# Kernel tuning notes

Measured on AMD Instinct MI355X. Metric: run time of the kernel, lower is better.

Reference implementation:

```python
import jax, jax.numpy as jnp
import numpy as np

WS = 8      # window size
S = 2       # num_heads
GRID = jnp.linspace(-2.0, 2.0, 8)  # RBF grid, num_grids=8
DENOM = 4.0 / 7.0                  # (grid_max-grid_min)/(num_grids-1)


def _layernorm(x, g, b, eps=1e-5):
    mu = x.mean(-1, keepdims=True)
    var = ((x - mu) ** 2).mean(-1, keepdims=True)
    return (x - mu) * jax.lax.rsqrt(var + eps) * g + b


def _fastkan(x, ln_g, ln_b, ws, wb, bb):
    # x: (..., in_dim). RBF basis: (..., in_dim, 8) -> flatten -> spline GEMM; plus SiLU base path.
    ln = _layernorm(x, ln_g, ln_b)
    basis = jnp.exp(-(((ln[..., None] - GRID) / DENOM) ** 2))
    flat = basis.reshape(*basis.shape[:-2], -1)
    return flat @ ws.T + jax.nn.silu(x) @ wb.T + bb


def setup_inputs() -> dict:
    key = jax.random.key(0)
    ks = jax.random.split(key, 16)
    d = {
        'x': jax.random.normal(ks[0], (4, 32, 256, 256), dtype=jnp.float32),
        'pn_g': jnp.ones((32,), jnp.float32), 'pn_b': jnp.zeros((32,), jnp.float32),
        'k1_ln_g': jnp.ones((16,), jnp.float32), 'k1_ln_b': jnp.zeros((16,), jnp.float32),
        'k1_ws': jax.random.normal(ks[1], (16, 128), jnp.float32) * 0.1,
        'k1_wb': jax.random.normal(ks[2], (16, 16), jnp.float32) * 0.1,
        'k1_bb': jnp.zeros((16,), jnp.float32),
        'k2_ln_g': jnp.ones((16,), jnp.float32), 'k2_ln_b': jnp.zeros((16,), jnp.float32),
        'k2_ws': jax.random.normal(ks[3], (16, 128), jnp.float32) * 0.1,
        'k2_wb': jax.random.normal(ks[4], (16, 16), jnp.float32) * 0.1,
        'k2_bb': jnp.zeros((16,), jnp.float32),
        'k3_ln_g': jnp.ones((32,), jnp.float32), 'k3_ln_b': jnp.zeros((32,), jnp.float32),
        'k3_ws': jax.random.normal(ks[5], (32, 256), jnp.float32) * 0.1,
        'k3_wb': jax.random.normal(ks[6], (32, 32), jnp.float32) * 0.1,
        'k3_bb': jnp.zeros((32,), jnp.float32),
        'k4_ln_g': jnp.ones((32,), jnp.float32), 'k4_ln_b': jnp.zeros((32,), jnp.float32),
        'k4_ws': jax.random.normal(ks[7], (32, 256), jnp.float32) * 0.1,
        'k4_wb': jax.random.normal(ks[8], (32, 32), jnp.float32) * 0.1,
        'k4_bb': jnp.zeros((32,), jnp.float32),
    }
    return d


def reference(x, pn_g, pn_b,
              k1_ln_g, k1_ln_b, k1_ws, k1_wb, k1_bb,
              k2_ln_g, k2_ln_b, k2_ws, k2_wb, k2_bb,
              k3_ln_g, k3_ln_b, k3_ws, k3_wb, k3_bb,
              k4_ln_g, k4_ln_b, k4_ws, k4_wb, k4_bb):
    B, C, H, W = x.shape
    c = C // S
    # b c h w -> b h w c, then window partition (shift_size=0, no padding)
    xh = jnp.transpose(x, (0, 2, 3, 1))
    wins = xh.reshape(B, H // WS, WS, W // WS, WS, C).transpose(0, 1, 3, 2, 4, 5).reshape(-1, WS, WS, C)
    b = wins.shape[0]
    # PreNormResidual
    y = _layernorm(wins, pn_g, pn_b)
    # branch 1: 'b h w (c s) -> b (w c) (h s)'
    a = y.reshape(b, WS, WS, c, S).transpose(0, 2, 3, 1, 4).reshape(b, WS * c, WS * S)
    a = _fastkan(a, k1_ln_g, k1_ln_b, k1_ws, k1_wb, k1_bb)
    a = a.reshape(b, WS, c, WS, S).transpose(0, 3, 1, 2, 4).reshape(b, WS, WS, C)
    # branch 2: 'b h w (c s) -> b (h c) (w s)'
    d = y.reshape(b, WS, WS, c, S).transpose(0, 1, 3, 2, 4).reshape(b, WS * c, WS * S)
    d = _fastkan(d, k2_ln_g, k2_ln_b, k2_ws, k2_wb, k2_bb)
    d = d.reshape(b, WS, c, WS, S).transpose(0, 1, 3, 2, 4).reshape(b, WS, WS, C)
    # branch 3: channel mixing
    e = _fastkan(y.reshape(b, WS * WS, C), k3_ln_g, k3_ln_b, k3_ws, k3_wb, k3_bb).reshape(b, WS, WS, C)
    z = a + d + e
    # output KAN layer then residual
    z = _fastkan(z.reshape(b, WS * WS, C), k4_ln_g, k4_ln_b, k4_ws, k4_wb, k4_bb).reshape(b, WS, WS, C)
    out = z + wins
    # window reverse, back to b c h w
    out = out.reshape(B, H // WS, W // WS, WS, WS, C).transpose(0, 1, 3, 2, 4, 5).reshape(B, H, W, C)
    return jnp.transpose(out, (0, 3, 1, 2))
```

## Files before the change

kernel.cpp:

```cpp
#include <hip/hip_runtime.h>

typedef __attribute__((ext_vector_type(8))) short  s8v;
typedef __attribute__((ext_vector_type(8))) __bf16 b8v;
typedef __attribute__((ext_vector_type(2))) __bf16 b2v;
typedef __attribute__((ext_vector_type(4))) float  f4v;
typedef __attribute__((ext_vector_type(2))) float  f2v;

#define LDST 36

#define WAVE_FENCE() do { asm volatile("s_waitcnt lgkmcnt(0)" ::: "memory"); \
                          __builtin_amdgcn_sched_barrier(0); } while(0)

#define W2_OFF 2560
#define W3_OFF 5120
#define W4_OFF 14336
#define W_TOTAL 23552
#define PREP_TOTAL (192 + W_TOTAL)

__device__ __forceinline__ float frcp_(float x){ return __builtin_amdgcn_rcpf(x); }
__device__ __forceinline__ float rsq_(float x){ return __builtin_amdgcn_rsqf(x); }
__device__ __forceinline__ float silu_(float x){ return x * frcp_(1.0f + __expf(-x)); }

__device__ __forceinline__ s8v b2s(b8v v){ union { b8v b; s8v s; } u; u.b = v; return u.s; }

__device__ __forceinline__ b8v basis8bf_(float u){
  float b = __expf(-u*u);
  float A = __expf(2.0f*u);
  b8v r;
  r[0] = (__bf16)b;
  b *= A * 0.36787944117144233f;   r[1] = (__bf16)b;
  b *= A * 0.049787068367863944f;  r[2] = (__bf16)b;
  b *= A * 0.006737946999085467f;  r[3] = (__bf16)b;
  b *= A * 0.0009118819655545162f; r[4] = (__bf16)b;
  b *= A * 1.2340980408667956e-4f; r[5] = (__bf16)b;
  b *= A * 1.670170079024566e-5f;  r[6] = (__bf16)b;
  b *= A * 2.2603294069810542e-6f; r[7] = (__bf16)b;
  return r;
}

__global__ void prep_w(const float* __restrict__ ws1, const float* __restrict__ wb1,
                       const float* __restrict__ ws2, const float* __restrict__ wb2,
                       const float* __restrict__ ws3, const float* __restrict__ wb3,
                       const float* __restrict__ ws4, const float* __restrict__ wb4,
                       const float* __restrict__ g1, const float* __restrict__ b1,
                       const float* __restrict__ g2, const float* __restrict__ b2,
                       const float* __restrict__ g3, const float* __restrict__ b3,
                       const float* __restrict__ g4, const float* __restrict__ b4,
                       float* __restrict__ LNP, __bf16* __restrict__ W){
  int idx = blockIdx.x*256 + threadIdx.x;
  if (idx >= PREP_TOTAL) return;
  if (idx < 192){
    float v;
    if      (idx < 16)  v = 1.75f * g1[idx];
    else if (idx < 32)  v = 1.75f * (b1[idx-16] + 2.0f);
    else if (idx < 48)  v = 1.75f * g2[idx-32];
    else if (idx < 64)  v = 1.75f * (b2[idx-48] + 2.0f);
    else if (idx < 96)  v = 1.75f * g3[idx-64];
    else if (idx < 128) v = 1.75f * (b3[idx-96] + 2.0f);
    else if (idx < 160) v = 1.75f * g4[idx-128];
    else                v = 1.75f * (b4[idx-160] + 2.0f);
    LNP[idx] = v;
    return;
  }
  int widx = idx - 192;
  float v;
  if (widx < W3_OFF){
    int base = (widx >= W2_OFF) ? W2_OFF : 0;
    const float* ws = base ? ws2 : ws1;
    const float* wb = base ? wb2 : wb1;
    int r = widx - base; int o = r/160, k = r%160;
    if (k < 128){
      int ks = k>>5, kg = (k>>3)&3, j = k&7;
      int elem = kg*4 + ks;
      v = ws[o*128 + elem*8 + j];
    } else {
      int kk = k-128; int kg = kk>>3, j = kk&7;
      v = (j<4) ? wb[o*16 + kg*4 + j] : 0.0f;
    }
  } else {
    int base = (widx >= W4_OFF) ? W4_OFF : W3_OFF;
    const float* ws = (base == W4_OFF) ? ws4 : ws3;
    const float* wb = (base == W4_OFF) ? wb4 : wb3;
    int r = widx - base; int o = r/288, k = r%288;
    if (k < 256){
      int ks = k>>5, kg = (k>>3)&3, j = k&7;
      int elem = kg*8 + ks;
      v = ws[o*256 + elem*8 + j];
    } else {
      int kk = k-256; int kg = kk>>3, j = kk&7;
      v = wb[o*32 + kg*8 + j];
    }
  }
  W[widx] = (__bf16)v;
}

__global__ __launch_bounds__(256,4)
void swin_kan_mfma(const float* __restrict__ x,
                   const float* __restrict__ pn_g, const float* __restrict__ pn_b,
                   const float* __restrict__ k1_bb, const float* __restrict__ k2_bb,
                   const float* __restrict__ k3_bb, const float* __restrict__ k4_bb,
                   const float* __restrict__ LNP,
                   const __bf16* __restrict__ Wbf,
                   float* __restrict__ out)
{
  __shared__ __attribute__((aligned(16))) float  yw[64][LDST];
  __shared__ __attribute__((aligned(16))) float  zA[64][LDST];
  __shared__ __attribute__((aligned(16))) float  LNPs[192];

  const int t   = threadIdx.x;
  const int bid = blockIdx.x;
  const int wid = (bid & 7)*512 + (bid >> 3);
  const int b   = wid >> 10;
  const int h0  = ((wid >> 5) & 31) * 8;
  const int w0  = (wid & 31) * 8;
  const int wave = t >> 6;
  const int lane = t & 63;
  const int fn = lane & 15, kg = lane >> 4;

  float4 xv0, xv1;

  {
    int ch = t & 31, h = t >> 5;
    const float* src = x + (((size_t)(b*32 + ch)*256 + (h0+h))*256 + w0);
    xv0 = *(const float4*)(src);
    xv1 = *(const float4*)(src + 4);
    int p = h*8;
    yw[p+0][ch]=xv0.x; yw[p+1][ch]=xv0.y; yw[p+2][ch]=xv0.z; yw[p+3][ch]=xv0.w;
    yw[p+4][ch]=xv1.x; yw[p+5][ch]=xv1.y; yw[p+6][ch]=xv1.z; yw[p+7][ch]=xv1.w;
    if (t < 192) LNPs[t] = LNP[t];
  }
  WAVE_FENCE();

  {
    int pos = t >> 2, part = t & 3;
    f4v a = *(const f4v*)&yw[pos][part*8];
    f4v c = *(const f4v*)&yw[pos][part*8+4];
    float s1 = a[0]+a[1]+a[2]+a[3]+c[0]+c[1]+c[2]+c[3];
    float s2 = a[0]*a[0]+a[1]*a[1]+a[2]*a[2]+a[3]*a[3]
             + c[0]*c[0]+c[1]*c[1]+c[2]*c[2]+c[3]*c[3];
    s1 += __shfl_xor(s1,1); s2 += __shfl_xor(s2,1);
    s1 += __shfl_xor(s1,2); s2 += __shfl_xor(s2,2);
    float mu  = s1*(1.0f/32.0f);
    float var = s2*(1.0f/32.0f) - mu*mu;
    float rs  = rsq_(var + 1e-5f);
    f4v g0 = *(const f4v*)&pn_g[part*8], g1 = *(const f4v*)&pn_g[part*8+4];
    f4v b0 = *(const f4v*)&pn_b[part*8], b1 = *(const f4v*)&pn_b[part*8+4];
    f4v o0, o1;
    #pragma unroll
    for (int j=0;j<4;j++){ o0[j] = (a[j]-mu)*rs*g0[j] + b0[j]; o1[j] = (c[j]-mu)*rs*g1[j] + b1[j]; }
    *(f4v*)&yw[pos][part*8]   = o0;
    *(f4v*)&yw[pos][part*8+4] = o1;
  }
  __syncthreads();

  {
    const bool br2 = (wave >= 2);
    const __bf16* Wp  = Wbf + (br2 ? W2_OFF : 0);
    const float* bbp = br2 ? k2_bb : k1_bb;
    const int gb = br2 ? 32 : 0, b2b = gb + 16;
    s8v wfr[5];
    #pragma unroll
    for (int ks=0;ks<5;ks++) wfr[ks] = *(const s8v*)&Wp[fn*160 + ks*32 + kg*8];
    f4v bias = *(const f4v*)&bbp[kg*4];
    f4v G  = *(const f4v*)&LNPs[gb  + kg*4];
    f4v B2 = *(const f4v*)&LNPs[b2b + kg*4];

    f4v accs[4];
    #pragma unroll
    for (int mi=0; mi<4; mi++){
      const int ck = (wave & 1)*4 + mi;
      const int posA = br2 ? (ck*8 + 2*kg) : ((2*kg)*8 + ck);
      const int posB = posA + (br2 ? 1 : 8);
      f2v va = *(const f2v*)&yw[posA][2*fn];
      f2v vb = *(const f2v*)&yw[posB][2*fn];
      float v[4] = { va[0], va[1], vb[0], vb[1] };
      b8v bb = {};
      #pragma unroll
      for (int j=0;j<4;j++) bb[j] = (__bf16)silu_(v[j]);

      float s1 = v[0]+v[1]+v[2]+v[3];
      float s2 = v[0]*v[0]+v[1]*v[1]+v[2]*v[2]+v[3]*v[3];
      s1 += __shfl_xor(s1,16); s2 += __shfl_xor(s2,16);
      s1 += __shfl_xor(s1,32); s2 += __shfl_xor(s2,32);
      float mu  = s1*(1.0f/16.0f);
      float var = s2*(1.0f/16.0f) - mu*mu;
      float rs  = rsq_(var + 1e-5f);

      f4v acc = bias;
      #pragma unroll
      for (int ks=0;ks<4;ks++){
        float pp = G[ks]*rs;
        float qq = __builtin_fmaf(-mu, pp, B2[ks]);
        float u  = __builtin_fmaf(v[ks], pp, qq);
        acc = __builtin_amdgcn_mfma_f32_16x16x32_bf16(wfr[ks], b2s(basis8bf_(u)), acc, 0,0,0);
      }
      acc = __builtin_amdgcn_mfma_f32_16x16x32_bf16(wfr[4], b2s(bb), acc, 0,0,0);
      accs[mi] = acc;
    }

    if (!br2){
      #pragma unroll
      for (int mi=0; mi<4; mi++){
        const int ck = (wave & 1)*4 + mi;
        *(f2v*)&zA[(2*kg+0)*8 + ck][2*fn] = f2v{accs[mi][0], accs[mi][1]};
        *(f2v*)&zA[(2*kg+1)*8 + ck][2*fn] = f2v{accs[mi][2], accs[mi][3]};
      }
    }
    __syncthreads();
    if (br2){
      #pragma unroll
      for (int mi=0; mi<4; mi++){
        const int ck = (wave & 1)*4 + mi;
        f2v o0 = *(f2v*)&zA[ck*8 + 2*kg+0][2*fn];
        f2v o1 = *(f2v*)&zA[ck*8 + 2*kg+1][2*fn];
        o0[0] += accs[mi][0]; o0[1] += accs[mi][1];
        o1[0] += accs[mi][2]; o1[1] += accs[mi][3];
        *(f2v*)&zA[ck*8 + 2*kg+0][2*fn] = o0;
        *(f2v*)&zA[ck*8 + 2*kg+1][2*fn] = o1;
      }
    }
  }
  __syncthreads();

  {
    const int r = wave*16 + fn;
    f4v v0 = *(const f4v*)&yw[r][kg*8];
    f4v v1 = *(const f4v*)&yw[r][kg*8+4];
    float v[8] = { v0[0],v0[1],v0[2],v0[3], v1[0],v1[1],v1[2],v1[3] };
    b8v bb;
    #pragma unroll
    for (int ks=0;ks<8;ks++) bb[ks] = (__bf16)silu_(v[ks]);
    float s1=0.f, s2=0.f;
    #pragma unroll
    for (int ks=0;ks<8;ks++){ s1 += v[ks]; s2 += v[ks]*v[ks]; }
    s1 += __shfl_xor(s1,16); s2 += __shfl_xor(s2,16);
    s1 += __shfl_xor(s1,32); s2 += __shfl_xor(s2,32);
    float mu  = s1*(1.0f/32.0f);
    float var = s2*(1.0f/32.0f) - mu*mu;
    float rs  = rsq_(var + 1e-5f);

    f4v Ga = *(const f4v*)&LNPs[64 + kg*8], Gb = *(const f4v*)&LNPs[64 + kg*8 + 4];
    f4v Ba = *(const f4v*)&LNPs[96 + kg*8], Bb = *(const f4v*)&LNPs[96 + kg*8 + 4];
    float G8[8]  = { Ga[0],Ga[1],Ga[2],Ga[3], Gb[0],Gb[1],Gb[2],Gb[3] };
    float B8[8]  = { Ba[0],Ba[1],Ba[2],Ba[3], Bb[0],Bb[1],Bb[2],Bb[3] };

    f4v acc0 = *(const f4v*)&k3_bb[kg*4];
    f4v acc1 = *(const f4v*)&k3_bb[16 + kg*4];
    #pragma unroll
    for (int ks=0;ks<8;ks++){
      float pp = G8[ks]*rs;
      float qq = __builtin_fmaf(-mu, pp, B8[ks]);
      float u  = __builtin_fmaf(v[ks], pp, qq);
      s8v bf = b2s(basis8bf_(u));
      s8v wa = *(const s8v*)&Wbf[W3_OFF + fn*288      + ks*32 + kg*8];
      s8v wb = *(const s8v*)&Wbf[W3_OFF + (16+fn)*288 + ks*32 + kg*8];
      acc0 = __builtin_amdgcn_mfma_f32_16x16x32_bf16(wa, bf, acc0, 0,0,0);
      acc1 = __builtin_amdgcn_mfma_f32_16x16x32_bf16(wb, bf, acc1, 0,0,0);
    }
    {
      s8v wa = *(const s8v*)&Wbf[W3_OFF + fn*288      + 256 + kg*8];
      s8v wb = *(const s8v*)&Wbf[W3_OFF + (16+fn)*288 + 256 + kg*8];
      acc0 = __builtin_amdgcn_mfma_f32_16x16x32_bf16(wa, b2s(bb), acc0, 0,0,0);
      acc1 = __builtin_amdgcn_mfma_f32_16x16x32_bf16(wb, b2s(bb), acc1, 0,0,0);
    }
    f4v za0 = *(const f4v*)&zA[r][kg*4];
    f4v za1 = *(const f4v*)&zA[r][16+kg*4];
    *(f4v*)&zA[r][kg*4]    = acc0 + za0;
    *(f4v*)&zA[r][16+kg*4] = acc1 + za1;
  }
  WAVE_FENCE();

  {
    const int r = wave*16 + fn;
    f4v v0 = *(const f4v*)&zA[r][kg*8];
    f4v v1 = *(const f4v*)&zA[r][kg*8+4];
    float v[8] = { v0[0],v0[1],v0[2],v0[3], v1[0],v1[1],v1[2],v1[3] };
    float s1=0.f, s2=0.f;
    #pragma unroll
    for (int ks=0;ks<8;ks++){ s1 += v[ks]; s2 += v[ks]*v[ks]; }
    s1 += __shfl_xor(s1,16); s2 += __shfl_xor(s2,16);
    s1 += __shfl_xor(s1,32); s2 += __shfl_xor(s2,32);
    float mu  = s1*(1.0f/32.0f);
    float var = s2*(1.0f/32.0f) - mu*mu;
    float rs  = rsq_(var + 1e-5f);

    f4v Ga = *(const f4v*)&LNPs[128 + kg*8], Gb = *(const f4v*)&LNPs[128 + kg*8 + 4];
    f4v Ba = *(const f4v*)&LNPs[160 + kg*8], Bb = *(const f4v*)&LNPs[160 + kg*8 + 4];
    float G8[8]  = { Ga[0],Ga[1],Ga[2],Ga[3], Gb[0],Gb[1],Gb[2],Gb[3] };
    float B8[8]  = { Ba[0],Ba[1],Ba[2],Ba[3], Bb[0],Bb[1],Bb[2],Bb[3] };

    f4v acc0 = *(const f4v*)&k4_bb[kg*4];
    f4v acc1 = *(const f4v*)&k4_bb[16 + kg*4];
    b8v bb;
    #pragma unroll
    for (int ks=0;ks<8;ks++){
      float pp = G8[ks]*rs;
      float qq = __builtin_fmaf(-mu, pp, B8[ks]);
      float u  = __builtin_fmaf(v[ks], pp, qq);
      s8v bf = b2s(basis8bf_(u));
      s8v wa = *(const s8v*)&Wbf[W4_OFF + fn*288      + ks*32 + kg*8];
      s8v wb = *(const s8v*)&Wbf[W4_OFF + (16+fn)*288 + ks*32 + kg*8];
      acc0 = __builtin_amdgcn_mfma_f32_16x16x32_bf16(wa, bf, acc0, 0,0,0);
      acc1 = __builtin_amdgcn_mfma_f32_16x16x32_bf16(wb, bf, acc1, 0,0,0);
      bb[ks] = (__bf16)silu_(v[ks]);
    }
    {
      s8v wa = *(const s8v*)&Wbf[W4_OFF + fn*288      + 256 + kg*8];
      s8v wb = *(const s8v*)&Wbf[W4_OFF + (16+fn)*288 + 256 + kg*8];
      acc0 = __builtin_amdgcn_mfma_f32_16x16x32_bf16(wa, b2s(bb), acc0, 0,0,0);
      acc1 = __builtin_amdgcn_mfma_f32_16x16x32_bf16(wb, b2s(bb), acc1, 0,0,0);
    }
    *(f4v*)&yw[r][kg*4]    = acc0;
    *(f4v*)&yw[r][16+kg*4] = acc1;
  }
  WAVE_FENCE();

  {
    int ch = t & 31, h = t >> 5;
    const size_t base = (((size_t)(b*32 + ch)*256 + (h0+h))*256 + w0);
    int p = h*8;
    float4 v0 = { yw[p+0][ch]+xv0.x, yw[p+1][ch]+xv0.y, yw[p+2][ch]+xv0.z, yw[p+3][ch]+xv0.w };
    float4 v1 = { yw[p+4][ch]+xv1.x, yw[p+5][ch]+xv1.y, yw[p+6][ch]+xv1.z, yw[p+7][ch]+xv1.w };
    *(float4*)(out + base)     = v0;
    *(float4*)(out + base + 4) = v1;
  }
}

extern "C" void kernel_launch(void* const* d_in, const int* in_sizes, int n_in,
                              void* d_out, int out_size, void* d_ws, size_t ws_size,
                              hipStream_t stream) {
  const float* x      = (const float*)d_in[0];
  const float* pn_g   = (const float*)d_in[1];
  const float* pn_b   = (const float*)d_in[2];
  const float* k1_ln_g= (const float*)d_in[3];
  const float* k1_ln_b= (const float*)d_in[4];
  const float* k1_ws  = (const float*)d_in[5];
  const float* k1_wb  = (const float*)d_in[6];
  const float* k1_bb  = (const float*)d_in[7];
  const float* k2_ln_g= (const float*)d_in[8];
  const float* k2_ln_b= (const float*)d_in[9];
  const float* k2_ws  = (const float*)d_in[10];
  const float* k2_wb  = (const float*)d_in[11];
  const float* k2_bb  = (const float*)d_in[12];
  const float* k3_ln_g= (const float*)d_in[13];
  const float* k3_ln_b= (const float*)d_in[14];
  const float* k3_ws  = (const float*)d_in[15];
  const float* k3_wb  = (const float*)d_in[16];
  const float* k3_bb  = (const float*)d_in[17];
  const float* k4_ln_g= (const float*)d_in[18];
  const float* k4_ln_b= (const float*)d_in[19];
  const float* k4_ws  = (const float*)d_in[20];
  const float* k4_wb  = (const float*)d_in[21];
  const float* k4_bb  = (const float*)d_in[22];
  float* out = (float*)d_out;
  float*  LNP = (float*)d_ws;
  __bf16* Wbf = (__bf16*)((char*)d_ws + 768);

  hipLaunchKernelGGL(prep_w, dim3((PREP_TOTAL+255)/256), dim3(256), 0, stream,
                     k1_ws, k1_wb, k2_ws, k2_wb, k3_ws, k3_wb, k4_ws, k4_wb,
                     k1_ln_g, k1_ln_b, k2_ln_g, k2_ln_b,
                     k3_ln_g, k3_ln_b, k4_ln_g, k4_ln_b,
                     LNP, Wbf);

  hipLaunchKernelGGL(swin_kan_mfma, dim3(4096), dim3(256), 0, stream,
                     x, pn_g, pn_b,
                     k1_bb, k2_bb, k3_bb, k4_bb,
                     LNP, Wbf, out);
}
```

Baseline: 67.65 us.

## Stage W3 weights in LDS via async global_load_lds and batch branch LN reductions

Copies the branch-3 bf16 weight block (18 KB) into shared memory with direct global-to-LDS loads issued during the input load phase, and reads the MFMA weight fragments from LDS instead of global memory. It also restructures the branch 1/2 loop so all four LayerNorm reductions are computed up front, giving the shuffles more instruction-level parallelism. Launch bounds drop from 4 to 3 blocks per SM, likely to fit the extra LDS, which may reduce occupancy. There is also a risk that the async LDS writes are not covered by the lgkmcnt-only fence, since global_load_lds completion is tracked through vmcnt.

```diff
diff --git a/kernel.cpp b/kernel.cpp
--- a/kernel.cpp
+++ b/kernel.cpp
@@ -2,7 +2,6 @@
 
 typedef __attribute__((ext_vector_type(8))) short  s8v;
 typedef __attribute__((ext_vector_type(8))) __bf16 b8v;
-typedef __attribute__((ext_vector_type(2))) __bf16 b2v;
 typedef __attribute__((ext_vector_type(4))) float  f4v;
 typedef __attribute__((ext_vector_type(2))) float  f2v;
 
@@ -22,6 +21,12 @@
 __device__ __forceinline__ float silu_(float x){ return x * frcp_(1.0f + __expf(-x)); }
 
 __device__ __forceinline__ s8v b2s(b8v v){ union { b8v b; s8v s; } u; u.b = v; return u.s; }
+
+__device__ __forceinline__ void gl_lds16(const void* g, void* l){
+  __builtin_amdgcn_global_load_lds(
+      (const __attribute__((address_space(1))) unsigned int*)g,
+      (__attribute__((address_space(3))) unsigned int*)l, 16, 0, 0);
+}
 
 __device__ __forceinline__ b8v basis8bf_(float u){
   float b = __expf(-u*u);
@@ -94,7 +99,7 @@
   W[widx] = (__bf16)v;
 }
 
-__global__ __launch_bounds__(256,4)
+__global__ __launch_bounds__(256,3)
 void swin_kan_mfma(const float* __restrict__ x,
                    const float* __restrict__ pn_g, const float* __restrict__ pn_b,
                    const float* __restrict__ k1_bb, const float* __restrict__ k2_bb,
@@ -106,6 +111,7 @@
   __shared__ __attribute__((aligned(16))) float  yw[64][LDST];
   __shared__ __attribute__((aligned(16))) float  zA[64][LDST];
   __shared__ __attribute__((aligned(16))) float  LNPs[192];
+  __shared__ __attribute__((aligned(16))) __bf16 W3s[9216];
 
   const int t   = threadIdx.x;
   const int bid = blockIdx.x;
@@ -128,6 +134,11 @@
     yw[p+0][ch]=xv0.x; yw[p+1][ch]=xv0.y; yw[p+2][ch]=xv0.z; yw[p+3][ch]=xv0.w;
     yw[p+4][ch]=xv1.x; yw[p+5][ch]=xv1.y; yw[p+6][ch]=xv1.z; yw[p+7][ch]=xv1.w;
     if (t < 192) LNPs[t] = LNP[t];
+    const char* gsrc  = (const char*)(Wbf + W3_OFF);
+    char*       lbase = (char*)W3s;
+    for (int c = wave; c < 18; c += 4){
+      gl_lds16(gsrc + c*1024 + lane*16, lbase + c*1024);
+    }
   }
   WAVE_FENCE();
 
@@ -165,32 +176,38 @@
     f4v G  = *(const f4v*)&LNPs[gb  + kg*4];
     f4v B2 = *(const f4v*)&LNPs[b2b + kg*4];
 
-    f4v accs[4];
+    f2v va[4], vb[4];
     #pragma unroll
     for (int mi=0; mi<4; mi++){
       const int ck = (wave & 1)*4 + mi;
       const int posA = br2 ? (ck*8 + 2*kg) : ((2*kg)*8 + ck);
       const int posB = posA + (br2 ? 1 : 8);
-      f2v va = *(const f2v*)&yw[posA][2*fn];
-      f2v vb = *(const f2v*)&yw[posB][2*fn];
-      float v[4] = { va[0], va[1], vb[0], vb[1] };
+      va[mi] = *(const f2v*)&yw[posA][2*fn];
+      vb[mi] = *(const f2v*)&yw[posB][2*fn];
+    }
+    float mu4[4], rs4[4];
+    #pragma unroll
+    for (int mi=0; mi<4; mi++){
+      float s1 = va[mi][0]+va[mi][1]+vb[mi][0]+vb[mi][1];
+      float s2 = va[mi][0]*va[mi][0]+va[mi][1]*va[mi][1]+vb[mi][0]*vb[mi][0]+vb[mi][1]*vb[mi][1];
+      s1 += __shfl_xor(s1,16); s2 += __shfl_xor(s2,16);
+      s1 += __shfl_xor(s1,32); s2 += __shfl_xor(s2,32);
+      float mu = s1*(1.0f/16.0f);
+      mu4[mi] = mu;
+      rs4[mi] = rsq_(s2*(1.0f/16.0f) - mu*mu + 1e-5f);
+    }
+    f4v accs[4];
+    #pragma unroll
+    for (int mi=0; mi<4; mi++){
+      float v[4] = { va[mi][0], va[mi][1], vb[mi][0], vb[mi][1] };
       b8v bb = {};
       #pragma unroll
       for (int j=0;j<4;j++) bb[j] = (__bf16)silu_(v[j]);
-
-      float s1 = v[0]+v[1]+v[2]+v[3];
-      float s2 = v[0]*v[0]+v[1]*v[1]+v[2]*v[2]+v[3]*v[3];
-      s1 += __shfl_xor(s1,16); s2 += __shfl_xor(s2,16);
-      s1 += __shfl_xor(s1,32); s2 += __shfl_xor(s2,32);
-      float mu  = s1*(1.0f/16.0f);
-      float var = s2*(1.0f/16.0f) - mu*mu;
-      float rs  = rsq_(var + 1e-5f);
-
       f4v acc = bias;
       #pragma unroll
       for (int ks=0;ks<4;ks++){
-        float pp = G[ks]*rs;
-        float qq = __builtin_fmaf(-mu, pp, B2[ks]);
+        float pp = G[ks]*rs4[mi];
+        float qq = __builtin_fmaf(-mu4[mi], pp, B2[ks]);
         float u  = __builtin_fmaf(v[ks], pp, qq);
         acc = __builtin_amdgcn_mfma_f32_16x16x32_bf16(wfr[ks], b2s(basis8bf_(u)), acc, 0,0,0);
       }
@@ -252,14 +269,14 @@
       float qq = __builtin_fmaf(-mu, pp, B8[ks]);
       float u  = __builtin_fmaf(v[ks], pp, qq);
       s8v bf = b2s(basis8bf_(u));
-      s8v wa = *(const s8v*)&Wbf[W3_OFF + fn*288      + ks*32 + kg*8];
-      s8v wb = *(const s8v*)&Wbf[W3_OFF + (16+fn)*288 + ks*32 + kg*8];
+      s8v wa = *(const s8v*)&W3s[fn*288      + ks*32 + kg*8];
+      s8v wb = *(const s8v*)&W3s[(16+fn)*288 + ks*32 + kg*8];
       acc0 = __builtin_amdgcn_mfma_f32_16x16x32_bf16(wa, bf, acc0, 0,0,0);
       acc1 = __builtin_amdgcn_mfma_f32_16x16x32_bf16(wb, bf, acc1, 0,0,0);
     }
     {
-      s8v wa = *(const s8v*)&Wbf[W3_OFF + fn*288      + 256 + kg*8];
-      s8v wb = *(const s8v*)&Wbf[W3_OFF + (16+fn)*288 + 256 + kg*8];
+      s8v wa = *(const s8v*)&W3s[fn*288      + 256 + kg*8];
+      s8v wb = *(const s8v*)&W3s[(16+fn)*288 + 256 + kg*8];
       acc0 = __builtin_amdgcn_mfma_f32_16x16x32_bf16(wa, b2s(bb), acc0, 0,0,0);
       acc1 = __builtin_amdgcn_mfma_f32_16x16x32_bf16(wb, b2s(bb), acc1, 0,0,0);
     }
```

After: 64.28 us. 5.0% less time.
